# Performance work log

Hardware: AMD Instinct MI355X
Metric: run time of the kernel (lower is better)

The kernel has to match this reference:

```python
import jax, jax.numpy as jnp
from jax import lax
import numpy as np

NUM_GRIDS = (40, 36, 24, 16, 12)
B, C = 4, 256
SMPL_OUT, CATE_OUT = 157, 1  # 24*6 pose + 10 shape + 3 cam; num_classes-1
SIZES = ((200, 200), (100, 100), (50, 50), (25, 25), (13, 13))


def setup_inputs():
    key = jax.random.key(0)
    ks = jax.random.split(key, 16)
    inp = {}
    for i, (h, w) in enumerate(SIZES):
        inp['feat%d' % i] = jax.random.normal(ks[i], (B, C, h, w), jnp.float32)
    def W(k, shape):
        return jax.random.normal(k, shape, jnp.float32) * 0.02
    inp['smpl_w0'] = W(ks[5], (C, C + 2, 3, 3)); inp['smpl_b0'] = jnp.zeros((C,), jnp.float32)
    inp['smpl_w'] = W(ks[6], (3, C, C, 3, 3)); inp['smpl_b'] = jnp.zeros((3, C), jnp.float32)
    inp['cate_w0'] = W(ks[7], (C, C, 3, 3)); inp['cate_b0'] = jnp.zeros((C,), jnp.float32)
    inp['cate_w'] = W(ks[8], (3, C, C, 3, 3)); inp['cate_b'] = jnp.zeros((3, C), jnp.float32)
    inp['cate_head_w'] = W(ks[9], (CATE_OUT, C, 3, 3)); inp['cate_head_b'] = jnp.zeros((CATE_OUT,), jnp.float32)
    inp['smpl_head_w'] = W(ks[10], (SMPL_OUT, C, 1, 1)); inp['smpl_head_b'] = jnp.zeros((SMPL_OUT,), jnp.float32)
    inp['smpl_init'] = W(ks[11], (SMPL_OUT,))  # stands in for init_contrep/shape/cam buffer
    return inp


def conv2d(x, w, b, pad):
    y = lax.conv_general_dilated(x, w, (1, 1), [(pad, pad), (pad, pad)],
                                 dimension_numbers=('NCHW', 'OIHW', 'NCHW'))
    return y + b[None, :, None, None]


def resize_ac(x, oh, ow):
    # bilinear resize, align_corners=True (matches F.interpolate(..., align_corners=True))
    H, W = x.shape[-2], x.shape[-1]
    ys = jnp.linspace(0.0, H - 1.0, oh)
    xs = jnp.linspace(0.0, W - 1.0, ow)
    y0 = jnp.floor(ys).astype(jnp.int32); y1 = jnp.minimum(y0 + 1, H - 1)
    x0 = jnp.floor(xs).astype(jnp.int32); x1 = jnp.minimum(x0 + 1, W - 1)
    wy = (ys - y0)[:, None]; wx = xs - x0
    r0, r1 = x[..., y0, :], x[..., y1, :]
    top = r0[..., x0] * (1 - wx) + r0[..., x1] * wx
    bot = r1[..., x0] * (1 - wx) + r1[..., x1] * wx
    return top * (1 - wy) + bot * wy


def points_nms(heat):
    # max_pool2d(kernel=2, stride=1, pad=1) -> (H+1, W+1); compare on [:-1, :-1]
    hmax = lax.reduce_window(heat, -jnp.inf, lax.max, (1, 1, 2, 2), (1, 1, 1, 1),
                             [(0, 0), (0, 0), (1, 1), (1, 1)])[:, :, :-1, :-1]
    return heat * (hmax == heat).astype(heat.dtype)


def _forward(feats, p):
    # split_feats: downsample P2 by 0.5, upsample P6 to P5 size (both align_corners bilinear)
    f0 = resize_ac(feats[0], feats[0].shape[-2] // 2, feats[0].shape[-1] // 2)
    f4 = resize_ac(feats[4], feats[3].shape[-2], feats[3].shape[-1])
    new_feats = (f0, feats[1], feats[2], feats[3], f4)
    smpl_outs, cate_outs = [], []
    for idx, x in enumerate(new_feats):
        g = NUM_GRIDS[idx]
        b, _, h, w = x.shape
        xr = jnp.linspace(-1.0, 1.0, w); yr = jnp.linspace(-1.0, 1.0, h)
        yy, xx = jnp.meshgrid(yr, xr, indexing='ij')
        coord = jnp.broadcast_to(jnp.stack([xx, yy])[None], (b, 2, h, w))  # CoordConv
        smpl_feat = resize_ac(jnp.concatenate([x, coord], axis=1), g, g)
        cate_feat = resize_ac(x, g, g)
        smpl_feat = jax.nn.relu(conv2d(smpl_feat, p['smpl_w0'], p['smpl_b0'], 1))
        cate_feat = jax.nn.relu(conv2d(cate_feat, p['cate_w0'], p['cate_b0'], 1))
        for i in range(3):  # remaining stacked convs (weights shared across levels)
            smpl_feat = jax.nn.relu(conv2d(smpl_feat, p['smpl_w'][i], p['smpl_b'][i], 1))
            cate_feat = jax.nn.relu(conv2d(cate_feat, p['cate_w'][i], p['cate_b'][i], 1))
        cate_pred = conv2d(cate_feat, p['cate_head_w'], p['cate_head_b'], 1)
        smpl_pred = conv2d(smpl_feat, p['smpl_head_w'], p['smpl_head_b'], 0) \
                    + p['smpl_init'][None, :, None, None]
        # eval=True branch: points-NMS on sigmoid heatmap, NHWC permute
        cate_pred = points_nms(jax.nn.sigmoid(cate_pred)).transpose(0, 2, 3, 1)
        smpl_pred = smpl_pred.transpose(0, 2, 3, 1)
        smpl_outs.append(smpl_pred); cate_outs.append(cate_pred)
    return tuple(smpl_outs) + tuple(cate_outs)


def reference(feat0, feat1, feat2, feat3, feat4, smpl_w0, smpl_b0, smpl_w, smpl_b,
              cate_w0, cate_b0, cate_w, cate_b, cate_head_w, cate_head_b,
              smpl_head_w, smpl_head_b, smpl_init):
    p = dict(smpl_w0=smpl_w0, smpl_b0=smpl_b0, smpl_w=smpl_w, smpl_b=smpl_b,
             cate_w0=cate_w0, cate_b0=cate_b0, cate_w=cate_w, cate_b=cate_b,
             cate_head_w=cate_head_w, cate_head_b=cate_head_b,
             smpl_head_w=smpl_head_w, smpl_head_b=smpl_head_b, smpl_init=smpl_init)
    return _forward((feat0, feat1, feat2, feat3, feat4), p)
```

## Files before the change

### kernel.cpp

```cpp
#include <hip/hip_runtime.h>
#include <math.h>
#include <stdint.h>

#define NLEV 5
#define PPT 17616
#define HPX 320

typedef __attribute__((ext_vector_type(8))) __bf16 bf16x8;
typedef __attribute__((ext_vector_type(4))) float f32x4;
typedef unsigned int u32;
typedef unsigned short u16;

#define MFMA16 __builtin_amdgcn_mfma_f32_16x16x32_bf16

__device__ __forceinline__ u32 f2bf(float f) {
  u32 u = __builtin_bit_cast(u32, f);
  return (u + 0x7FFFu + ((u >> 16) & 1u)) >> 16;
}
__device__ __forceinline__ void split2(float v, u32& hi, u32& lo) {
  hi = f2bf(v);
  lo = f2bf(v - __builtin_bit_cast(float, hi << 16));
}
__device__ __forceinline__ float bf2f(u32 bits16) {
  return __builtin_bit_cast(float, bits16 << 16);
}


struct PrepDesc {
  const float* src[9];
  int Cin[9];
  int Cout[9];
  int CB[9];
  int TAPS[9];
  int nCoT[9];
  int dstOff[9];
};

__global__ __launch_bounds__(256) void prep_weights(PrepDesc pd, u16* __restrict__ wHi,
                                                    u16* __restrict__ wLo) {
  int cfg = blockIdx.y;
  int CB = pd.CB[cfg];
  int TAPS = pd.TAPS[cfg];
  int KS = CB * TAPS;
  int total = KS * 2048 * pd.nCoT[cfg];
  int didx = blockIdx.x * 256 + threadIdx.x;
  if (didx >= total) return;
  int j = didx & 7;
  int lane = (didx >> 3) & 63;
  int wco = (didx >> 9) & 1;
  int f = (didx >> 10) & 1;
  int rest = didx >> 11;
  int ks = rest % KS;
  int coT = rest / KS;
  int cb = ks / TAPS;
  int tap = ks - cb * TAPS;
  int ci = cb * 32 + ((lane >> 4) << 3) + j;
  int co = coT * 64 + wco * 32 + f * 16 + (lane & 15);
  float v = 0.f;
  if (ci < pd.Cin[cfg] && co < pd.Cout[cfg])
    v = pd.src[cfg][((size_t)co * pd.Cin[cfg] + ci) * TAPS + tap];
  u32 hi, lo;
  split2(v, hi, lo);
  wHi[pd.dstOff[cfg] + didx] = (u16)hi;
  wLo[pd.dstOff[cfg] + didx] = (u16)lo;
}

struct ZeroDesc {
  int padOff[NLEV];
  int g[NLEV];
};

__global__ __launch_bounds__(256) void halo_zero(u16* __restrict__ base, ZeroDesc zd) {
  int px = blockIdx.x * 256 + threadIdx.x;
  if (px >= PPT) return;
  int l = 0;
#pragma unroll
  for (int i = 1; i < NLEV; i++)
    if (px >= zd.padOff[i]) l = i;
  int g = zd.g[l], gp2 = g + 2, hp2 = gp2 * gp2;
  int local = px - zd.padOff[l];
  int b = local / hp2;
  int rem = local - b * hp2;
  int yy = rem / gp2, xx = rem - yy * gp2;
  if (yy >= 1 && yy <= g && xx >= 1 && xx <= g) return;
  int r = blockIdx.y;
  uint4 z = {0u, 0u, 0u, 0u};
  *(uint4*)(base + ((size_t)r * PPT + px) * 8) = z;
}

struct BuildDesc {
  const float* src[NLEV];
  int H[NLEV];
  int mid[NLEV];
  int P[NLEV];
  int g[NLEV];
  int padOff[NLEV];
};

__device__ __forceinline__ float bsample(const float* __restrict__ pl, int H, int W,
                                         float fy, float fx) {
  int y0 = (int)floorf(fy);
  int y1 = min(y0 + 1, H - 1);
  float wy = fy - (float)y0;
  int x0 = (int)floorf(fx);
  int x1 = min(x0 + 1, W - 1);
  float wx = fx - (float)x0;
  const float* r0 = pl + (size_t)y0 * W;
  const float* r1 = pl + (size_t)y1 * W;
  float top = r0[x0] * (1.f - wx) + r0[x1] * wx;
  float bot = r1[x0] * (1.f - wx) + r1[x1] * wx;
  return top * (1.f - wy) + bot * wy;
}

__global__ __launch_bounds__(256) void build_all(BuildDesc bd, u16* __restrict__ dst) {
  int l = blockIdx.y;
  int P = bd.P[l];
  int g = bd.g[l];
  int total = 258 * P;
  int idx = blockIdx.x * 256 + threadIdx.x;
  if (idx >= total) return;
  int c = idx / P;
  int p = idx - c * P;
  int gg = g * g;
  int b = p / gg;
  int pr = p - b * gg;
  int i = pr / g;
  int j = pr - i * g;
  float val;
  if (c >= 256) {
    int tt = (c == 256) ? j : i;
    val = -1.f + 2.f * (float)tt / (float)(g - 1);
  } else {
    int H = bd.H[l], W = bd.H[l];
    int mid = bd.mid[l];
    const float* pl = bd.src[l] + ((size_t)b * 256 + c) * H * W;
    if (!mid) {
      float fy = (float)i * (float)(H - 1) / (float)(g - 1);
      float fx = (float)j * (float)(W - 1) / (float)(g - 1);
      val = bsample(pl, H, W, fy, fx);
    } else {
      int midh = mid, midw = mid;
      float fym = (float)i * (float)(midh - 1) / (float)(g - 1);
      float fxm = (float)j * (float)(midw - 1) / (float)(g - 1);
      int y0 = (int)floorf(fym);
      int y1 = min(y0 + 1, midh - 1);
      float wy = fym - (float)y0;
      int x0 = (int)floorf(fxm);
      int x1 = min(x0 + 1, midw - 1);
      float wx = fxm - (float)x0;
      float sy0 = (float)y0 * (float)(H - 1) / (float)(midh - 1);
      float sy1 = (float)y1 * (float)(H - 1) / (float)(midh - 1);
      float sx0 = (float)x0 * (float)(W - 1) / (float)(midw - 1);
      float sx1 = (float)x1 * (float)(W - 1) / (float)(midw - 1);
      float v00 = bsample(pl, H, W, sy0, sx0);
      float v01 = bsample(pl, H, W, sy0, sx1);
      float v10 = bsample(pl, H, W, sy1, sx0);
      float v11 = bsample(pl, H, W, sy1, sx1);
      float top = v00 * (1.f - wx) + v01 * wx;
      float bot = v10 * (1.f - wx) + v11 * wx;
      val = top * (1.f - wy) + bot * wy;
    }
  }
  int gp2 = g + 2;
  int hpos = bd.padOff[l] + b * gp2 * gp2 + (i + 1) * gp2 + (j + 1);
  u32 hi, lo;
  split2(val, hi, lo);
  size_t base = ((size_t)(c >> 3) * PPT + hpos) * 8 + (c & 7);
  dst[base] = (u16)hi;
  dst[(size_t)36 * PPT * 8 + base] = (u16)lo;
}

struct ConvDesc {
  int tS[NLEV + 1];
  int padOff[NLEV];
  int g[NLEV];
  int P[NLEV];
};

__global__ __launch_bounds__(256) void conv_mfma(
    const u16* __restrict__ inS, const u16* __restrict__ inC, int inCRows,
    const u16* __restrict__ wHiB, const u16* __restrict__ wLoB, int wOffS,
    int wOffC, const float* __restrict__ bS, const float* __restrict__ bC,
    u16* __restrict__ outS, u16* __restrict__ outC, ConvDesc d, int CBS, int CBC) {
  const int bid = blockIdx.x;
  const int xcd = bid & 7;
  const int i6 = bid >> 3;
  const int tower = i6 & 1;
  const int coT = (i6 >> 1) & 3;
  const int tile = xcd + (i6 >> 3) * 8;
  if (tile >= d.tS[NLEV]) return;

  const bool dual = (tower != 0);
  const u16* __restrict__ inHi = tower ? inC : inS;
  const u16* __restrict__ inLo = inHi + (size_t)inCRows * PPT * 8;
  u16* __restrict__ outHi = tower ? outC : outS;
  u16* __restrict__ outLo = outHi + (size_t)32 * PPT * 8;
  const u16* __restrict__ wH = wHiB + (tower ? wOffC : wOffS);
  const u16* __restrict__ wL = wLoB + (tower ? wOffC : wOffS);
  const float* __restrict__ bias = tower ? bC : bS;
  const int CB = tower ? CBC : CBS;
  const int KS = CB * 9;

  int l = 0;
#pragma unroll
  for (int i = 1; i < NLEV; i++)
    if (tile >= d.tS[i]) l = i;
  const int g = d.g[l];
  const int gp2 = g + 2, hp2 = gp2 * gp2, gg = g * g;
  const int padOff = d.padOff[l];
  const int Pl = d.P[l];
  const int ptile = (tile - d.tS[l]) * 128;

  const int t = threadIdx.x;
  const int lane = t & 63;
  const int wv = t >> 6;
  const int wco = wv & 1, wp = wv >> 1;
  const int kb = lane >> 4;
  const int sgr = wv;

  int h0;
  {
    int b0 = ptile / gg, pr0 = ptile - b0 * gg;
    int y0 = pr0 / g, x0 = pr0 - y0 * g;
    h0 = padOff + b0 * hp2 + (y0 + 1) * gp2 + (x0 + 1) - gp2 - 1;
  }

  int hRel[4], ob[4];
  bool vst[4];
#pragma unroll
  for (int fi = 0; fi < 4; fi++) {
    int pb = ptile + wp * 64 + fi * 16;
    vst[fi] = pb < Pl;
    int pf = pb + (lane & 15);
    if (pf >= Pl) pf = Pl - 1;
    int b = pf / gg, pr = pf - b * gg;
    int y = pr / g, x = pr - y * g;
    int h = padOff + b * hp2 + (y + 1) * gp2 + (x + 1);
    hRel[fi] = h - h0;
    ob[fi] = h;
  }

  __shared__ u16 halo[2 * 4 * 2 * HPX * 8];

  f32x4 acc[2][4];
#pragma unroll
  for (int c = 0; c < 2; c++)
#pragma unroll
    for (int fi = 0; fi < 4; fi++) acc[c][fi] = (f32x4){0.f, 0.f, 0.f, 0.f};

  const size_t wbase =
      (size_t)coT * KS * 2048 + (size_t)wco * 512 + (size_t)lane * 8;
  bf16x8 ah0 = *(const bf16x8*)(wH + wbase);
  bf16x8 ah1 = *(const bf16x8*)(wH + wbase + 1024);
  bf16x8 al0 = *(const bf16x8*)(wL + wbase);
  bf16x8 al1 = *(const bf16x8*)(wL + wbase + 1024);

#define STAGE(dbuf, cbn)                                                          \
  {                                                                               \
    const int gr_ = (cbn)*4 + sgr;                                                \
    const u16* ghi_ = inHi + ((size_t)gr_ * PPT + h0) * 8;                        \
    u16* lb_ = halo + (size_t)(((dbuf)*4 + sgr) * 2) * (HPX * 8);                 \
    _Pragma("unroll") for (int i_ = 0; i_ < 5; i_++) {                            \
      __builtin_amdgcn_global_load_lds(                                           \
          (const __attribute__((address_space(1))) void*)(ghi_ +                  \
                                                          (size_t)(i_ * 64 + lane) * 8), \
          (__attribute__((address_space(3))) void*)(lb_ + i_ * 64 * 8), 16, 0, 0);\
    }                                                                             \
    if (dual) {                                                                   \
      const u16* glo_ = inLo + ((size_t)gr_ * PPT + h0) * 8;                      \
      _Pragma("unroll") for (int i_ = 0; i_ < 5; i_++) {                          \
        __builtin_amdgcn_global_load_lds(                                         \
            (const __attribute__((address_space(1))) void*)(glo_ +                \
                                                            (size_t)(i_ * 64 + lane) * 8), \
            (__attribute__((address_space(3))) void*)(lb_ + HPX * 8 +             \
                                                      i_ * 64 * 8),               \
            16, 0, 0);                                                            \
      }                                                                           \
    }                                                                             \
  }

  STAGE(0, 0);

  for (int cb = 0; cb < CB; ++cb) {
    const int cur = cb & 1;
    __syncthreads();
    if (cb + 1 < CB) STAGE(cur ^ 1, cb + 1);

#pragma unroll
    for (int tap = 0; tap < 9; ++tap) {
      const int ks = cb * 9 + tap;
      bf16x8 ah0n, ah1n, al0n, al1n;
      const bool have = (ks + 1) < KS;
      if (have) {
        size_t wo = wbase + (size_t)(ks + 1) * 2048;
        ah0n = *(const bf16x8*)(wH + wo);
        ah1n = *(const bf16x8*)(wH + wo + 1024);
        al0n = *(const bf16x8*)(wL + wo);
        al1n = *(const bf16x8*)(wL + wo + 1024);
      }
      const int toff = (tap / 3 - 1) * gp2 + (tap % 3) - 1;
      const u16* kbase = halo + (size_t)((cur * 4 + kb) * 2) * (HPX * 8);
#pragma unroll
      for (int fi = 0; fi < 4; fi++) {
        const u16* p0 = kbase + (hRel[fi] + toff) * 8;
        bf16x8 bh = *(const bf16x8*)p0;
        acc[0][fi] = MFMA16(ah0, bh, acc[0][fi], 0, 0, 0);
        acc[0][fi] = MFMA16(al0, bh, acc[0][fi], 0, 0, 0);
        acc[1][fi] = MFMA16(ah1, bh, acc[1][fi], 0, 0, 0);
        acc[1][fi] = MFMA16(al1, bh, acc[1][fi], 0, 0, 0);
        if (dual) {
          bf16x8 bl = *(const bf16x8*)(p0 + HPX * 8);
          acc[0][fi] = MFMA16(ah0, bl, acc[0][fi], 0, 0, 0);
          acc[1][fi] = MFMA16(ah1, bl, acc[1][fi], 0, 0, 0);
        }
      }
      if (have) {
        ah0 = ah0n;
        ah1 = ah1n;
        al0 = al0n;
        al1 = al1n;
      }
    }
  }
#undef STAGE

  const int coBase = coT * 64 + wco * 32 + ((lane >> 4) << 2);
  float bAv[4], bBv[4];
#pragma unroll
  for (int i = 0; i < 4; i++) {
    bAv[i] = bias[coBase + i];
    bBv[i] = bias[coBase + 16 + i];
  }
  const size_t rowA = (size_t)(coBase >> 3) * PPT;
  const size_t rowB = (size_t)((coBase + 16) >> 3) * PPT;
  const int sub = coBase & 7;
#pragma unroll
  for (int fi = 0; fi < 4; fi++) {
    if (!vst[fi]) continue;
    if (!dual) {
      u32 h[4];
#pragma unroll
      for (int i = 0; i < 4; i++) h[i] = f2bf(fmaxf(acc[0][fi][i] + bAv[i], 0.f));
      uint2 hs = {h[0] | (h[1] << 16), h[2] | (h[3] << 16)};
      *(uint2*)(outHi + (rowA + ob[fi]) * 8 + sub) = hs;
#pragma unroll
      for (int i = 0; i < 4; i++) h[i] = f2bf(fmaxf(acc[1][fi][i] + bBv[i], 0.f));
      hs.x = h[0] | (h[1] << 16);
      hs.y = h[2] | (h[3] << 16);
      *(uint2*)(outHi + (rowB + ob[fi]) * 8 + sub) = hs;
    } else {
      u32 h[4], lo[4];
#pragma unroll
      for (int i = 0; i < 4; i++)
        split2(fmaxf(acc[0][fi][i] + bAv[i], 0.f), h[i], lo[i]);
      uint2 hs = {h[0] | (h[1] << 16), h[2] | (h[3] << 16)};
      uint2 ls = {lo[0] | (lo[1] << 16), lo[2] | (lo[3] << 16)};
      *(uint2*)(outHi + (rowA + ob[fi]) * 8 + sub) = hs;
      *(uint2*)(outLo + (rowA + ob[fi]) * 8 + sub) = ls;
#pragma unroll
      for (int i = 0; i < 4; i++)
        split2(fmaxf(acc[1][fi][i] + bBv[i], 0.f), h[i], lo[i]);
      hs.x = h[0] | (h[1] << 16);
      hs.y = h[2] | (h[3] << 16);
      ls.x = lo[0] | (lo[1] << 16);
      ls.y = lo[2] | (lo[3] << 16);
      *(uint2*)(outHi + (rowB + ob[fi]) * 8 + sub) = hs;
      *(uint2*)(outLo + (rowB + ob[fi]) * 8 + sub) = ls;
    }
  }
}

struct HeadDesc {
  int tS64[NLEV + 1];
  int padOff[NLEV];
  int g[NLEV];
  int outOff[NLEV];
};

__global__ __launch_bounds__(256) void head1x1(
    const u16* __restrict__ actIn, const u16* __restrict__ wH,
    const u16* __restrict__ wL, const float* __restrict__ bias,
    const float* __restrict__ bias2, float* __restrict__ outB, HeadDesc d) {
  const int bx = blockIdx.x;
  const int coT = blockIdx.y;
  int l = 0;
#pragma unroll
  for (int i = 1; i < NLEV; i++)
    if (bx >= d.tS64[i]) l = i;
  const int g = d.g[l], gp2 = g + 2, hp2 = gp2 * gp2, gg = g * g;
  const int ptile = (bx - d.tS64[l]) * 64;
  const int t = threadIdx.x, lane = t & 63, wv = t >> 6;
  const int wco = wv & 1, wp = wv >> 1, kb = lane >> 4;

  int hp[2], pF[2];
#pragma unroll
  for (int fi = 0; fi < 2; fi++) {
    int pf = ptile + wp * 32 + fi * 16 + (lane & 15);
    pF[fi] = pf;
    int b = pf / gg, pr = pf - b * gg, y = pr / g, x = pr - y * g;
    hp[fi] = d.padOff[l] + b * hp2 + (y + 1) * gp2 + (x + 1);
  }
  f32x4 acc[2][2];
#pragma unroll
  for (int c = 0; c < 2; c++)
#pragma unroll
    for (int fi = 0; fi < 2; fi++) acc[c][fi] = (f32x4){0.f, 0.f, 0.f, 0.f};

  const size_t wbase = (size_t)coT * 8 * 2048 + (size_t)wco * 512 + (size_t)lane * 8;
  for (int cb = 0; cb < 8; ++cb) {
    size_t wo = wbase + (size_t)cb * 2048;
    bf16x8 ah0 = *(const bf16x8*)(wH + wo);
    bf16x8 ah1 = *(const bf16x8*)(wH + wo + 1024);
    bf16x8 al0 = *(const bf16x8*)(wL + wo);
    bf16x8 al1 = *(const bf16x8*)(wL + wo + 1024);
    const int gr = cb * 4 + kb;
#pragma unroll
    for (int fi = 0; fi < 2; fi++) {
      bf16x8 b = *(const bf16x8*)(actIn + ((size_t)gr * PPT + hp[fi]) * 8);
      acc[0][fi] = MFMA16(ah0, b, acc[0][fi], 0, 0, 0);
      acc[0][fi] = MFMA16(al0, b, acc[0][fi], 0, 0, 0);
      acc[1][fi] = MFMA16(ah1, b, acc[1][fi], 0, 0, 0);
      acc[1][fi] = MFMA16(al1, b, acc[1][fi], 0, 0, 0);
    }
  }
  const int coBase = coT * 64 + wco * 32 + ((lane >> 4) << 2);
#pragma unroll
  for (int c = 0; c < 2; c++)
#pragma unroll
    for (int fi = 0; fi < 2; fi++)
#pragma unroll
      for (int i = 0; i < 4; i++) {
        int co = coBase + c * 16 + i;
        if (co < 157)
          outB[d.outOff[l] + (size_t)pF[fi] * 157 + co] =
              acc[c][fi][i] + bias[co] + bias2[co];
      }
}

struct CHDesc {
  int tS64[NLEV + 1];
  int padOff[NLEV];
  int g[NLEV];
  int outOff[NLEV];
};

__global__ __launch_bounds__(256) void cate_head_all(
    const u16* __restrict__ inHi, const u16* __restrict__ inLo,
    const float* __restrict__ w, const float* __restrict__ bias,
    float* __restrict__ heat, CHDesc d) {
  int tile = blockIdx.x;
  int l = 0;
#pragma unroll
  for (int i = 1; i < NLEV; i++)
    if (tile >= d.tS64[i]) l = i;
  const int g = d.g[l];
  const int gp2 = g + 2, hp2 = gp2 * gp2, gg = g * g;
  const int t = threadIdx.x;
  const int ps = t & 63;
  const int cw = t >> 6;
  const int ptile = (tile - d.tS64[l]) * 64;
  int p = ptile + ps;
  int b = p / gg, pr = p - b * gg, y = pr / g, x = pr - y * g;
  const int hbase = d.padOff[l] + b * hp2 + (y + 1) * gp2 + (x + 1);

  __shared__ float ws[32][9][8];
  for (int i = t; i < 2304; i += 256) {
    int ci = i / 9, tap = i - ci * 9;
    ws[ci >> 3][tap][ci & 7] = w[i];
  }
  __syncthreads();

  float s = 0.f;
  for (int gr = cw; gr < 32; gr += 4) {
    const u16* ph = inHi + ((size_t)gr * PPT + hbase) * 8;
    const u16* pl = inLo + ((size_t)gr * PPT + hbase) * 8;
#pragma unroll
    for (int tap = 0; tap < 9; tap++) {
      const int toff = (tap / 3 - 1) * gp2 + (tap % 3) - 1;
      uint4 hq = *(const uint4*)(ph + (ptrdiff_t)toff * 8);
      uint4 lq = *(const uint4*)(pl + (ptrdiff_t)toff * 8);
      const float* wp = ws[gr][tap];
      s += (bf2f(hq.x & 0xFFFFu) + bf2f(lq.x & 0xFFFFu)) * wp[0] +
           (bf2f(hq.x >> 16) + bf2f(lq.x >> 16)) * wp[1] +
           (bf2f(hq.y & 0xFFFFu) + bf2f(lq.y & 0xFFFFu)) * wp[2] +
           (bf2f(hq.y >> 16) + bf2f(lq.y >> 16)) * wp[3] +
           (bf2f(hq.z & 0xFFFFu) + bf2f(lq.z & 0xFFFFu)) * wp[4] +
           (bf2f(hq.z >> 16) + bf2f(lq.z >> 16)) * wp[5] +
           (bf2f(hq.w & 0xFFFFu) + bf2f(lq.w & 0xFFFFu)) * wp[6] +
           (bf2f(hq.w >> 16) + bf2f(lq.w >> 16)) * wp[7];
    }
  }
  __shared__ float red[4][64];
  red[cw][ps] = s;
  __syncthreads();
  if (cw == 0) {
    float tot = bias[0] + red[0][ps] + red[1][ps] + red[2][ps] + red[3][ps];
    heat[d.outOff[l] + p] = 1.f / (1.f + expf(-tot));
  }
}

struct SmallDesc {
  int P[NLEV];
  int g[NLEV];
  int inOff[NLEV];
  int outOff[NLEV];
};

__global__ void nms_all(const float* __restrict__ heat, float* __restrict__ out,
                        SmallDesc d) {
  int l = blockIdx.y;
  int P = d.P[l], g = d.g[l];
  int gg = g * g;
  int p = blockIdx.x * 256 + threadIdx.x;
  if (p >= P) return;
  int pr = p % gg;
  int y = pr / g;
  int x = pr - y * g;
  const float* hb = heat + d.inOff[l];
  float c = hb[p], m = c;
  if (y > 0) {
    m = fmaxf(m, hb[p - g]);
    if (x > 0) m = fmaxf(m, hb[p - g - 1]);
  }
  if (x > 0) m = fmaxf(m, hb[p - 1]);
  out[d.outOff[l] + p] = (m == c) ? c : 0.f;
}

extern "C" void kernel_launch(void* const* d_in, const int* in_sizes, int n_in,
                              void* d_out, int out_size, void* d_ws, size_t ws_size,
                              hipStream_t stream) {
  const float* feat[5];
  for (int i = 0; i < 5; i++) feat[i] = (const float*)d_in[i];
  const float* smpl_w0 = (const float*)d_in[5];
  const float* smpl_b0 = (const float*)d_in[6];
  const float* smpl_w = (const float*)d_in[7];
  const float* smpl_b = (const float*)d_in[8];
  const float* cate_w0 = (const float*)d_in[9];
  const float* cate_b0 = (const float*)d_in[10];
  const float* cate_w = (const float*)d_in[11];
  const float* cate_b = (const float*)d_in[12];
  const float* cate_head_w = (const float*)d_in[13];
  const float* cate_head_b = (const float*)d_in[14];
  const float* smpl_head_w = (const float*)d_in[15];
  const float* smpl_head_b = (const float*)d_in[16];
  const float* smpl_init = (const float*)d_in[17];
  float* out = (float*)d_out;

  static const int GR[5] = {40, 36, 24, 16, 12};
  static const int SH[5] = {200, 100, 50, 25, 13};
  static const int MIDW[5] = {100, 0, 0, 0, 25};

  int P[5], cumP[6], tS64[6], tS128[6], padOff[5];
  cumP[0] = 0;
  tS64[0] = 0;
  tS128[0] = 0;
  int po = 0;
  for (int l = 0; l < 5; l++) {
    P[l] = 4 * GR[l] * GR[l];
    cumP[l + 1] = cumP[l] + P[l];
    tS64[l + 1] = tS64[l] + P[l] / 64;
    tS128[l + 1] = tS128[l] + (P[l] + 127) / 128;
    padOff[l] = po;
    po += 4 * (GR[l] + 2) * (GR[l] + 2);
  }

  int smpl_off[5], cate_off[5];
  {
    int off = 0;
    for (int l = 0; l < 5; l++) {
      smpl_off[l] = off;
      off += P[l] * 157;
    }
    for (int l = 0; l < 5; l++) {
      cate_off[l] = off;
      off += P[l];
    }
  }

  u16* bufA = (u16*)d_ws;
  u16* bufBs = bufA + (size_t)72 * PPT * 8;
  u16* bufCs = bufBs + (size_t)32 * PPT * 8;
  u16* bufBc = bufCs + (size_t)32 * PPT * 8;
  u16* bufCc = bufBc + (size_t)64 * PPT * 8;
  float* heat = (float*)(bufCc + (size_t)64 * PPT * 8);
  u16* wHi = (u16*)(heat + 15488);

  PrepDesc pd;
  const size_t LSTR = (size_t)256 * 256 * 9;
  pd.src[0] = smpl_w0;
  pd.src[1] = smpl_w;
  pd.src[2] = smpl_w + LSTR;
  pd.src[3] = smpl_w + 2 * LSTR;
  pd.src[4] = cate_w0;
  pd.src[5] = cate_w;
  pd.src[6] = cate_w + LSTR;
  pd.src[7] = cate_w + 2 * LSTR;
  pd.src[8] = smpl_head_w;
  for (int i = 0; i < 9; i++) {
    pd.Cin[i] = 256;
    pd.Cout[i] = 256;
    pd.CB[i] = 8;
    pd.TAPS[i] = 9;
    pd.nCoT[i] = 4;
  }
  pd.Cin[0] = 258;
  pd.CB[0] = 9;
  pd.Cout[8] = 157;
  pd.TAPS[8] = 1;
  pd.nCoT[8] = 3;
  size_t WTOT = 0;
  for (int i = 0; i < 9; i++) {
    pd.dstOff[i] = (int)WTOT;
    WTOT += (size_t)pd.CB[i] * pd.TAPS[i] * 2048 * pd.nCoT[i];
  }
  u16* wLo = wHi + WTOT;

  hipMemsetAsync(bufA, 0, (size_t)72 * PPT * 16, stream);
  ZeroDesc zd;
  for (int l = 0; l < 5; l++) {
    zd.padOff[l] = padOff[l];
    zd.g[l] = GR[l];
  }
  hipLaunchKernelGGL(halo_zero, dim3((PPT + 255) / 256, 192), dim3(256), 0, stream,
                     bufBs, zd);

  hipLaunchKernelGGL(prep_weights, dim3(2592, 9), dim3(256), 0, stream, pd, wHi, wLo);

  BuildDesc bd;
  for (int l = 0; l < 5; l++) {
    bd.src[l] = feat[l];
    bd.H[l] = SH[l];
    bd.mid[l] = MIDW[l];
    bd.P[l] = P[l];
    bd.g[l] = GR[l];
    bd.padOff[l] = padOff[l];
  }
  hipLaunchKernelGGL(build_all, dim3((258 * P[0] + 255) / 256, 5), dim3(256), 0,
                     stream, bd, bufA);

  ConvDesc cd;
  HeadDesc hd;
  CHDesc chd;
  SmallDesc nd;
  for (int i = 0; i <= 5; i++) {
    cd.tS[i] = tS128[i];
    hd.tS64[i] = tS64[i];
    chd.tS64[i] = tS64[i];
  }
  for (int l = 0; l < 5; l++) {
    cd.padOff[l] = padOff[l];
    cd.g[l] = GR[l];
    cd.P[l] = P[l];
    hd.padOff[l] = padOff[l];
    hd.g[l] = GR[l];
    hd.outOff[l] = smpl_off[l];
    chd.padOff[l] = padOff[l];
    chd.g[l] = GR[l];
    chd.outOff[l] = cumP[l];
    nd.P[l] = P[l];
    nd.g[l] = GR[l];
    nd.inOff[l] = cumP[l];
    nd.outOff[l] = cate_off[l];
  }

  const int NT64 = tS64[5];
  const int CGRID = 8 * 128;
  hipLaunchKernelGGL(conv_mfma, dim3(CGRID), dim3(256), 0, stream, bufA, bufA, 36,
                     wHi, wLo, pd.dstOff[0], pd.dstOff[4], smpl_b0, cate_b0, bufBs,
                     bufBc, cd, 9, 8);
  hipLaunchKernelGGL(conv_mfma, dim3(CGRID), dim3(256), 0, stream, bufBs, bufBc, 32,
                     wHi, wLo, pd.dstOff[1], pd.dstOff[5], smpl_b + 0, cate_b + 0,
                     bufCs, bufCc, cd, 8, 8);
  hipLaunchKernelGGL(conv_mfma, dim3(CGRID), dim3(256), 0, stream, bufCs, bufCc, 32,
                     wHi, wLo, pd.dstOff[2], pd.dstOff[6], smpl_b + 256,
                     cate_b + 256, bufBs, bufBc, cd, 8, 8);
  hipLaunchKernelGGL(conv_mfma, dim3(CGRID), dim3(256), 0, stream, bufBs, bufBc, 32,
                     wHi, wLo, pd.dstOff[3], pd.dstOff[7], smpl_b + 512,
                     cate_b + 512, bufCs, bufCc, cd, 8, 8);
  hipLaunchKernelGGL(head1x1, dim3(NT64, 3), dim3(256), 0, stream, bufCs,
                     wHi + pd.dstOff[8], wLo + pd.dstOff[8], smpl_head_b, smpl_init,
                     out, hd);
  hipLaunchKernelGGL(cate_head_all, dim3(NT64), dim3(256), 0, stream, bufCc,
                     bufCc + (size_t)32 * PPT * 8, cate_head_w, cate_head_b, heat,
                     chd);
  hipLaunchKernelGGL(nms_all, dim3((P[0] + 255) / 256, 5), dim3(256), 0, stream,
                     heat, out, nd);
  (void)in_sizes;
  (void)n_in;
  (void)out_size;
  (void)ws_size;
}
```

Before: 500.6 us.

## Remap conv waves to cover all 64 output channels over 32 pixels each

Changes the per-wave work split in the 3x3 conv kernel. Previously each of four waves handled 32 output channels by 64 pixels; now each wave handles all 64 channels by 32 pixels. Each LDS activation fragment is now reused across four channel fragments instead of two, which halves LDS reads per MFMA. The cost is doubling the per-wave weight fragment loads from global memory and holding more weight registers.

Measured after the change: 536.3 us. 7.1% more time.

```diff
diff --git a/kernel.cpp b/kernel.cpp
--- a/kernel.cpp
+++ b/kernel.cpp
@@ -214,7 +214,6 @@
   const int t = threadIdx.x;
   const int lane = t & 63;
   const int wv = t >> 6;
-  const int wco = wv & 1, wp = wv >> 1;
   const int kb = lane >> 4;
   const int sgr = wv;
 
@@ -225,11 +224,11 @@
     h0 = padOff + b0 * hp2 + (y0 + 1) * gp2 + (x0 + 1) - gp2 - 1;
   }
 
-  int hRel[4], ob[4];
-  bool vst[4];
-#pragma unroll
-  for (int fi = 0; fi < 4; fi++) {
-    int pb = ptile + wp * 64 + fi * 16;
+  int hRel[2], ob[2];
+  bool vst[2];
+#pragma unroll
+  for (int fi = 0; fi < 2; fi++) {
+    int pb = ptile + wv * 32 + fi * 16;
     vst[fi] = pb < Pl;
     int pf = pb + (lane & 15);
     if (pf >= Pl) pf = Pl - 1;
@@ -242,18 +241,21 @@
 
   __shared__ u16 halo[2 * 4 * 2 * HPX * 8];
 
-  f32x4 acc[2][4];
-#pragma unroll
-  for (int c = 0; c < 2; c++)
-#pragma unroll
-    for (int fi = 0; fi < 4; fi++) acc[c][fi] = (f32x4){0.f, 0.f, 0.f, 0.f};
-
-  const size_t wbase =
-      (size_t)coT * KS * 2048 + (size_t)wco * 512 + (size_t)lane * 8;
-  bf16x8 ah0 = *(const bf16x8*)(wH + wbase);
+  f32x4 acc[4][2];
+#pragma unroll
+  for (int cf = 0; cf < 4; cf++)
+#pragma unroll
+    for (int fi = 0; fi < 2; fi++) acc[cf][fi] = (f32x4){0.f, 0.f, 0.f, 0.f};
+
+  const size_t wbase = (size_t)coT * KS * 2048 + (size_t)lane * 8;
+  bf16x8 ah0 = *(const bf16x8*)(wH + wbase + 0);
   bf16x8 ah1 = *(const bf16x8*)(wH + wbase + 1024);
-  bf16x8 al0 = *(const bf16x8*)(wL + wbase);
+  bf16x8 ah2 = *(const bf16x8*)(wH + wbase + 512);
+  bf16x8 ah3 = *(const bf16x8*)(wH + wbase + 1536);
+  bf16x8 al0 = *(const bf16x8*)(wL + wbase + 0);
   bf16x8 al1 = *(const bf16x8*)(wL + wbase + 1024);
+  bf16x8 al2 = *(const bf16x8*)(wL + wbase + 512);
+  bf16x8 al3 = *(const bf16x8*)(wL + wbase + 1536);
 
 #define STAGE(dbuf, cbn)                                                          \
   {                                                                               \
@@ -289,83 +291,78 @@
 #pragma unroll
     for (int tap = 0; tap < 9; ++tap) {
       const int ks = cb * 9 + tap;
-      bf16x8 ah0n, ah1n, al0n, al1n;
+      bf16x8 ah0n, ah1n, ah2n, ah3n, al0n, al1n, al2n, al3n;
       const bool have = (ks + 1) < KS;
       if (have) {
         size_t wo = wbase + (size_t)(ks + 1) * 2048;
-        ah0n = *(const bf16x8*)(wH + wo);
+        ah0n = *(const bf16x8*)(wH + wo + 0);
         ah1n = *(const bf16x8*)(wH + wo + 1024);
-        al0n = *(const bf16x8*)(wL + wo);
+        ah2n = *(const bf16x8*)(wH + wo + 512);
+        ah3n = *(const bf16x8*)(wH + wo + 1536);
+        al0n = *(const bf16x8*)(wL + wo + 0);
         al1n = *(const bf16x8*)(wL + wo + 1024);
+        al2n = *(const bf16x8*)(wL + wo + 512);
+        al3n = *(const bf16x8*)(wL + wo + 1536);
       }
       const int toff = (tap / 3 - 1) * gp2 + (tap % 3) - 1;
       const u16* kbase = halo + (size_t)((cur * 4 + kb) * 2) * (HPX * 8);
 #pragma unroll
-      for (int fi = 0; fi < 4; fi++) {
+      for (int fi = 0; fi < 2; fi++) {
         const u16* p0 = kbase + (hRel[fi] + toff) * 8;
         bf16x8 bh = *(const bf16x8*)p0;
         acc[0][fi] = MFMA16(ah0, bh, acc[0][fi], 0, 0, 0);
         acc[0][fi] = MFMA16(al0, bh, acc[0][fi], 0, 0, 0);
         acc[1][fi] = MFMA16(ah1, bh, acc[1][fi], 0, 0, 0);
         acc[1][fi] = MFMA16(al1, bh, acc[1][fi], 0, 0, 0);
+        acc[2][fi] = MFMA16(ah2, bh, acc[2][fi], 0, 0, 0);
+        acc[2][fi] = MFMA16(al2, bh, acc[2][fi], 0, 0, 0);
+        acc[3][fi] = MFMA16(ah3, bh, acc[3][fi], 0, 0, 0);
+        acc[3][fi] = MFMA16(al3, bh, acc[3][fi], 0, 0, 0);
         if (dual) {
           bf16x8 bl = *(const bf16x8*)(p0 + HPX * 8);
           acc[0][fi] = MFMA16(ah0, bl, acc[0][fi], 0, 0, 0);
           acc[1][fi] = MFMA16(ah1, bl, acc[1][fi], 0, 0, 0);
+          acc[2][fi] = MFMA16(ah2, bl, acc[2][fi], 0, 0, 0);
+          acc[3][fi] = MFMA16(ah3, bl, acc[3][fi], 0, 0, 0);
         }
       }
       if (have) {
-        ah0 = ah0n;
-        ah1 = ah1n;
-        al0 = al0n;
-        al1 = al1n;
+        ah0 = ah0n; ah1 = ah1n; ah2 = ah2n; ah3 = ah3n;
+        al0 = al0n; al1 = al1n; al2 = al2n; al3 = al3n;
       }
     }
   }
 #undef STAGE
 
-  const int coBase = coT * 64 + wco * 32 + ((lane >> 4) << 2);
-  float bAv[4], bBv[4];
-#pragma unroll
-  for (int i = 0; i < 4; i++) {
-    bAv[i] = bias[coBase + i];
-    bBv[i] = bias[coBase + 16 + i];
-  }
-  const size_t rowA = (size_t)(coBase >> 3) * PPT;
-  const size_t rowB = (size_t)((coBase + 16) >> 3) * PPT;
-  const int sub = coBase & 7;
-#pragma unroll
-  for (int fi = 0; fi < 4; fi++) {
-    if (!vst[fi]) continue;
-    if (!dual) {
-      u32 h[4];
-#pragma unroll
-      for (int i = 0; i < 4; i++) h[i] = f2bf(fmaxf(acc[0][fi][i] + bAv[i], 0.f));
-      uint2 hs = {h[0] | (h[1] << 16), h[2] | (h[3] << 16)};
-      *(uint2*)(outHi + (rowA + ob[fi]) * 8 + sub) = hs;
-#pragma unroll
-      for (int i = 0; i < 4; i++) h[i] = f2bf(fmaxf(acc[1][fi][i] + bBv[i], 0.f));
-      hs.x = h[0] | (h[1] << 16);
-      hs.y = h[2] | (h[3] << 16);
-      *(uint2*)(outHi + (rowB + ob[fi]) * 8 + sub) = hs;
-    } else {
-      u32 h[4], lo[4];
-#pragma unroll
-      for (int i = 0; i < 4; i++)
-        split2(fmaxf(acc[0][fi][i] + bAv[i], 0.f), h[i], lo[i]);
-      uint2 hs = {h[0] | (h[1] << 16), h[2] | (h[3] << 16)};
-      uint2 ls = {lo[0] | (lo[1] << 16), lo[2] | (lo[3] << 16)};
-      *(uint2*)(outHi + (rowA + ob[fi]) * 8 + sub) = hs;
-      *(uint2*)(outLo + (rowA + ob[fi]) * 8 + sub) = ls;
-#pragma unroll
-      for (int i = 0; i < 4; i++)
-        split2(fmaxf(acc[1][fi][i] + bBv[i], 0.f), h[i], lo[i]);
-      hs.x = h[0] | (h[1] << 16);
-      hs.y = h[2] | (h[3] << 16);
-      ls.x = lo[0] | (lo[1] << 16);
-      ls.y = lo[2] | (lo[3] << 16);
-      *(uint2*)(outHi + (rowB + ob[fi]) * 8 + sub) = hs;
-      *(uint2*)(outLo + (rowB + ob[fi]) * 8 + sub) = ls;
+  const int coRow = (lane >> 4) << 2;
+#pragma unroll
+  for (int cf = 0; cf < 4; cf++) {
+    const int coStart = coT * 64 + cf * 16 + coRow;
+    float bv[4];
+#pragma unroll
+    for (int i = 0; i < 4; i++) bv[i] = bias[coStart + i];
+    const size_t row = (size_t)(coStart >> 3) * PPT;
+    const int sub = coStart & 7;
+#pragma unroll
+    for (int fi = 0; fi < 2; fi++) {
+      if (!vst[fi]) continue;
+      if (!dual) {
+        u32 h[4];
+#pragma unroll
+        for (int i = 0; i < 4; i++)
+          h[i] = f2bf(fmaxf(acc[cf][fi][i] + bv[i], 0.f));
+        uint2 hs = {h[0] | (h[1] << 16), h[2] | (h[3] << 16)};
+        *(uint2*)(outHi + (row + ob[fi]) * 8 + sub) = hs;
+      } else {
+        u32 h[4], lo[4];
+#pragma unroll
+        for (int i = 0; i < 4; i++)
+          split2(fmaxf(acc[cf][fi][i] + bv[i], 0.f), h[i], lo[i]);
+        uint2 hs = {h[0] | (h[1] << 16), h[2] | (h[3] << 16)};
+        uint2 ls = {lo[0] | (lo[1] << 16), lo[2] | (lo[3] << 16)};
+        *(uint2*)(outHi + (row + ob[fi]) * 8 + sub) = hs;
+        *(uint2*)(outLo + (row + ob[fi]) * 8 + sub) = ls;
+      }
     }
   }
 }
```
